# Kernel tuning notes

Hardware: AMD Instinct MI355X
Metric: run time of the kernel (lower is better)

## Reference

```python
import jax, jax.numpy as jnp
import numpy as np
from jax import lax

K_SIZE = 3
STRIDE = 1
PAD = 1
BN_EPS = 1e-5


def _unfold(x, k, stride, pad):
    # x: [B, C, H, W] -> patches [B, L, C*k*k] with torch.unfold feature
    # ordering (channel-major: feat = c*k*k + i*k + j), L = oH*oW
    B, C, H, W = x.shape
    xp = jnp.pad(x, ((0, 0), (0, 0), (pad, pad), (pad, pad)))
    oH = (H + 2 * pad - k) // stride + 1
    oW = (W + 2 * pad - k) // stride + 1
    views = []
    for i in range(k):
        for j in range(k):
            views.append(xp[:, :, i:i + oH * stride:stride, j:j + oW * stride:stride])
    p = jnp.stack(views, axis=0)            # [k*k, B, C, oH, oW]
    p = p.transpose(1, 3, 4, 2, 0)          # [B, oH, oW, C, k*k]
    return p.reshape(B, oH * oW, C * k * k), oH, oW


def _nearest_l1(flat, cents):
    # Online nearest-centroid search under L1, avoids [N, K] x D blowup.
    # flat: [N, D], cents: [K, D] -> int32 indices [N] (first min on ties,
    # matching torch argmin)
    N = flat.shape[0]
    init = (jnp.full((N,), jnp.inf, flat.dtype), jnp.zeros((N,), jnp.int32))
    ks = jnp.arange(cents.shape[0], dtype=jnp.int32)

    def body(carry, kc):
        kidx, c = kc
        d = jnp.abs(flat - c).sum(-1)       # [N]
        bd, bi = carry
        better = d < bd
        return (jnp.where(better, d, bd), jnp.where(better, kidx, bi)), None

    (_, best_idx), _ = lax.scan(body, init, (ks, cents))
    return best_idx


def setup_inputs() -> dict:
    key = jax.random.key(0)
    ks = jax.random.split(key, 5)
    B, Cin, H, W = 8, 64, 56, 56
    K, D, Cout = 256, Cin * K_SIZE * K_SIZE, 128
    return {
        "x": jax.random.normal(ks[0], (B, Cin, H, W), jnp.float32),
        "centroids": jax.random.normal(ks[1], (K, D), jnp.float32),
        "residual_centroids": jax.random.normal(ks[2], (K, D), jnp.float32),
        "dot_centroids": jax.random.normal(ks[3], (K, Cout), jnp.float32),
        "dot_residual_centroids": jax.random.normal(ks[4], (K, Cout), jnp.float32),
        "bn_gamma": jnp.ones((Cout,), jnp.float32),
        "bn_beta": jnp.zeros((Cout,), jnp.float32),
    }


def reference(x, centroids, residual_centroids, dot_centroids,
              dot_residual_centroids, bn_gamma, bn_beta):
    B = x.shape[0]
    Cout = dot_centroids.shape[1]
    patches, oH, oW = _unfold(x, K_SIZE, STRIDE, PAD)   # [B, L, D]
    L, D = patches.shape[1], patches.shape[2]
    flat = patches.reshape(B * L, D)

    # Stage 1: nearest centroid (L1)
    idx1 = _nearest_l1(flat, centroids)                  # [B*L]
    residuals = flat - centroids[idx1]                   # [B*L, D]
    # Stage 2: nearest residual centroid (L1)
    idx2 = _nearest_l1(residuals, residual_centroids)    # [B*L]

    # LUT gather + sum
    out_vals = dot_centroids[idx1] + dot_residual_centroids[idx2]  # [B*L, Cout]
    out = out_vals.reshape(B, L, Cout).transpose(0, 2, 1).reshape(B, Cout, oH, oW)

    # BatchNorm2d (training mode: biased batch statistics)
    mean = out.mean(axis=(0, 2, 3), keepdims=True)
    var = ((out - mean) ** 2).mean(axis=(0, 2, 3), keepdims=True)
    out = (out - mean) * lax.rsqrt(var + BN_EPS)
    out = out * bn_gamma[None, :, None, None] + bn_beta[None, :, None, None]
    return out
```

## Files before the change

### kernel.cpp

```cpp
#include <hip/hip_runtime.h>

#define NP 25088
#define DD 576
#define KC 256

__global__ __launch_bounds__(256) void unfold_kernel(const float* __restrict__ x,
                                                     float* __restrict__ PT) {
  const int d = blockIdx.y;
  const int n = blockIdx.x * 256 + threadIdx.x;
  const int c = d / 9, r = d % 9;
  const int di = r / 3 - 1, dj = r % 3 - 1;
  const int b = n / 3136, hw = n % 3136;
  const int h = hw / 56 + di, w = hw % 56 + dj;
  float v = 0.0f;
  if (h >= 0 && h < 56 && w >= 0 && w < 56)
    v = x[(((size_t)b * 64 + c) * 56 + h) * 56 + w];
  PT[(size_t)d * NP + n] = v;
}

__global__ __launch_bounds__(256) void transpose_kernel(const float* __restrict__ C,
                                                        float* __restrict__ CT) {
  const int d = blockIdx.x;
  const int k = threadIdx.x;
  CT[d * KC + k] = C[k * DD + d];
}

#define ACC4(p, a, s) \
  do { p.x += fabsf(a.x - (s)); p.y += fabsf(a.y - (s)); \
       p.z += fabsf(a.z - (s)); p.w += fabsf(a.w - (s)); } while (0)
#define ADD4(t, p) \
  do { t.x += p.x; t.y += p.y; t.z += p.z; t.w += p.w; } while (0)
#define COMP(v, i) ((i) == 0 ? (v).x : (i) == 1 ? (v).y : (i) == 2 ? (v).z : (v).w)

__global__ __launch_bounds__(256, 5) void nearest_kernel(const float* __restrict__ AT,
                                                         const float* __restrict__ CT,
                                                         float* __restrict__ distc,
                                                         int* __restrict__ idxc) {
  __shared__ float As[2][32][64];
  __shared__ float Bs[2][32][64];

  const int tid = threadIdx.x;
  const int tm = tid >> 4;
  const int tk = tid & 15;
  const int L = blockIdx.x;
  const int xcd = L & 7, r = L >> 3;
  const int mb = xcd * 49 + (r >> 2);
  const int kc = r & 3;
  const int m0 = mb * 64, k0 = kc * 64;

  float4 ra0, ra1, rb0, rb1;
  float4 p0, p1, p2, p3, t0, t1, t2, t3;

  const int frow = tid >> 4, fcol = (tid & 15) * 4;
  const float* ap = AT + (size_t)frow * NP + m0 + fcol;
  const float* bp = CT + frow * KC + k0 + fcol;

#define LOADT() do {                                       \
    ra0 = *(const float4*)(ap);                            \
    ra1 = *(const float4*)(ap + (size_t)16 * NP);          \
    rb0 = *(const float4*)(bp);                            \
    rb1 = *(const float4*)(bp + 16 * KC);                  \
    ap += (size_t)32 * NP; bp += 32 * KC;                  \
  } while (0)

#define WRITET(bf) do {                                    \
    *(float4*)&As[bf][frow][fcol] = ra0;                   \
    *(float4*)&As[bf][16 + frow][fcol] = ra1;              \
    *(float4*)&Bs[bf][frow][fcol] = rb0;                   \
    *(float4*)&Bs[bf][16 + frow][fcol] = rb1;              \
  } while (0)

  LOADT();
  WRITET(0);
  t0 = t1 = t2 = t3 = make_float4(0.f, 0.f, 0.f, 0.f);

  for (int ch = 0; ch < 18; ++ch) {
    if ((ch & 1) == 0) p0 = p1 = p2 = p3 = make_float4(0.f, 0.f, 0.f, 0.f);
    __syncthreads();
    if (ch < 17) LOADT();
    const int buf = ch & 1;
#pragma unroll 8
    for (int d = 0; d < 32; ++d) {
      const float4 a = *(const float4*)&As[buf][d][tm * 4];
      const float4 b = *(const float4*)&Bs[buf][d][tk * 4];
      ACC4(p0, a, b.x);
      ACC4(p1, a, b.y);
      ACC4(p2, a, b.z);
      ACC4(p3, a, b.w);
    }
    if (ch < 17) WRITET((ch + 1) & 1);
    if (ch & 1) {
      ADD4(t0, p0); ADD4(t1, p1); ADD4(t2, p2); ADD4(t3, p3);
    }
  }

#pragma unroll
  for (int i = 0; i < 4; ++i) {
    const float d0 = COMP(t0, i), d1 = COMP(t1, i), d2 = COMP(t2, i), d3 = COMP(t3, i);
    float bd = d0;
    int bk = k0 + tk * 4;
    if (d1 < bd) { bd = d1; bk = k0 + tk * 4 + 1; }
    if (d2 < bd) { bd = d2; bk = k0 + tk * 4 + 2; }
    if (d3 < bd) { bd = d3; bk = k0 + tk * 4 + 3; }
#pragma unroll
    for (int off = 1; off < 16; off <<= 1) {
      const float od = __shfl_xor(bd, off, 64);
      const int ok = __shfl_xor(bk, off, 64);
      if (od < bd || (od == bd && ok < bk)) { bd = od; bk = ok; }
    }
    if (tk == 0) {
      const int m = m0 + tm * 4 + i;
      distc[(size_t)kc * NP + m] = bd;
      idxc[(size_t)kc * NP + m] = bk;
    }
  }
#undef LOADT
#undef WRITET
}

__global__ __launch_bounds__(256) void combine_kernel(const float* __restrict__ distc,
                                                      const int* __restrict__ idxc,
                                                      int* __restrict__ idx_out) {
  const int n = blockIdx.x * 256 + threadIdx.x;
  if (n >= NP) return;
  float bd = distc[n];
  int bi = idxc[n];
#pragma unroll
  for (int s = 1; s < 4; ++s) {
    const float d = distc[(size_t)s * NP + n];
    if (d < bd) { bd = d; bi = idxc[(size_t)s * NP + n]; }
  }
  idx_out[n] = bi;
}

__global__ __launch_bounds__(256) void resid_kernel(float* __restrict__ PT,
                                                    const float* __restrict__ C1T,
                                                    const int* __restrict__ idx1) {
  const int d = blockIdx.y;
  const int n = blockIdx.x * 256 + threadIdx.x;
  const int k = idx1[n];
  PT[(size_t)d * NP + n] -= C1T[d * KC + k];
}

__global__ __launch_bounds__(256) void stats_kernel(const int* __restrict__ idx1,
                                                    const int* __restrict__ idx2,
                                                    const float* __restrict__ dotc,
                                                    const float* __restrict__ dotrc,
                                                    float* __restrict__ gsum,
                                                    float* __restrict__ gsq) {
  __shared__ float ssum[4][128], ssq[4][128];
  const int tid = threadIdx.x, lane = tid & 63, wv = tid >> 6;
  const int wid = blockIdx.x * 4 + wv;
  float s0 = 0.f, s1 = 0.f, q0 = 0.f, q1 = 0.f;
  for (int n = wid; n < NP; n += 512) {
    const int k1 = idx1[n], k2 = idx2[n];
    const float2 u = ((const float2*)(dotc + (size_t)k1 * 128))[lane];
    const float2 v = ((const float2*)(dotrc + (size_t)k2 * 128))[lane];
    const float x0 = u.x + v.x, x1 = u.y + v.y;
    s0 += x0; s1 += x1; q0 += x0 * x0; q1 += x1 * x1;
  }
  ssum[wv][lane * 2] = s0; ssum[wv][lane * 2 + 1] = s1;
  ssq[wv][lane * 2] = q0;  ssq[wv][lane * 2 + 1] = q1;
  __syncthreads();
  if (tid < 128) {
    const float s = ssum[0][tid] + ssum[1][tid] + ssum[2][tid] + ssum[3][tid];
    const float q = ssq[0][tid] + ssq[1][tid] + ssq[2][tid] + ssq[3][tid];
    atomicAdd(&gsum[tid], s);
    atomicAdd(&gsq[tid], q);
  }
}

__global__ void finalize_kernel(const float* __restrict__ gsum,
                                const float* __restrict__ gsq,
                                const float* __restrict__ gamma,
                                const float* __restrict__ beta,
                                float* __restrict__ scalev,
                                float* __restrict__ shiftv) {
  const int c = threadIdx.x;
  const float mean = gsum[c] * (1.0f / NP);
  const float var = gsq[c] * (1.0f / NP) - mean * mean;
  const float inv = rsqrtf(var + 1e-5f);
  const float sc = gamma[c] * inv;
  scalev[c] = sc;
  shiftv[c] = beta[c] - mean * sc;
}

__global__ __launch_bounds__(256) void output_kernel(const int* __restrict__ idx1,
                                                     const int* __restrict__ idx2,
                                                     const float* __restrict__ dotc,
                                                     const float* __restrict__ dotrc,
                                                     const float* __restrict__ scalev,
                                                     const float* __restrict__ shiftv,
                                                     float* __restrict__ out) {
  __shared__ float vals[64][128];
  const int tid = threadIdx.x, lane = tid & 63, wv = tid >> 6;
  const int blk = blockIdx.x;
  const int b = blk / 49, hw0 = (blk % 49) * 64;
  const int n0 = b * 3136 + hw0;
  const float sc0 = scalev[lane * 2], sc1 = scalev[lane * 2 + 1];
  const float sh0 = shiftv[lane * 2], sh1 = shiftv[lane * 2 + 1];
  for (int t = 0; t < 16; ++t) {
    const int nn = wv * 16 + t;
    const int n = n0 + nn;
    const int k1 = idx1[n], k2 = idx2[n];
    const float2 u = ((const float2*)(dotc + (size_t)k1 * 128))[lane];
    const float2 v = ((const float2*)(dotrc + (size_t)k2 * 128))[lane];
    *(float2*)&vals[nn][lane * 2] =
        make_float2(sc0 * (u.x + v.x) + sh0, sc1 * (u.y + v.y) + sh1);
  }
  __syncthreads();
  const int c = tid >> 1, half = tid & 1;
  float* op = out + ((size_t)b * 128 + c) * 3136 + hw0 + half * 32;
#pragma unroll
  for (int i = 0; i < 32; i += 4) {
    float4 w4;
    w4.x = vals[half * 32 + i + 0][c];
    w4.y = vals[half * 32 + i + 1][c];
    w4.z = vals[half * 32 + i + 2][c];
    w4.w = vals[half * 32 + i + 3][c];
    *(float4*)(op + i) = w4;
  }
}

extern "C" void kernel_launch(void* const* d_in, const int* in_sizes, int n_in,
                              void* d_out, int out_size, void* d_ws, size_t ws_size,
                              hipStream_t stream) {
  const float* x     = (const float*)d_in[0];
  const float* cent  = (const float*)d_in[1];
  const float* rcent = (const float*)d_in[2];
  const float* dotc  = (const float*)d_in[3];
  const float* dotrc = (const float*)d_in[4];
  const float* gamma = (const float*)d_in[5];
  const float* beta  = (const float*)d_in[6];
  float* out = (float*)d_out;

  float* PT  = (float*)d_ws;
  float* C1T = PT + (size_t)DD * NP;
  float* C2T = C1T + (size_t)DD * KC;
  int* idx1  = (int*)(C2T + (size_t)DD * KC);
  int* idx2  = idx1 + NP;
  float* distc = (float*)(idx2 + NP);
  int* idxc    = (int*)(distc + 4 * NP);
  float* gsum   = (float*)(idxc + 4 * NP);
  float* gsq    = gsum + 128;
  float* scalev = gsq + 128;
  float* shiftv = scalev + 128;

  unfold_kernel<<<dim3(98, 576), 256, 0, stream>>>(x, PT);
  transpose_kernel<<<576, 256, 0, stream>>>(cent, C1T);
  transpose_kernel<<<576, 256, 0, stream>>>(rcent, C2T);
  nearest_kernel<<<1568, 256, 0, stream>>>(PT, C1T, distc, idxc);
  combine_kernel<<<98, 256, 0, stream>>>(distc, idxc, idx1);
  resid_kernel<<<dim3(98, 576), 256, 0, stream>>>(PT, C1T, idx1);
  nearest_kernel<<<1568, 256, 0, stream>>>(PT, C2T, distc, idxc);
  combine_kernel<<<98, 256, 0, stream>>>(distc, idxc, idx2);
  hipMemsetAsync(gsum, 0, 256 * sizeof(float), stream);
  stats_kernel<<<128, 256, 0, stream>>>(idx1, idx2, dotc, dotrc, gsum, gsq);
  finalize_kernel<<<1, 128, 0, stream>>>(gsum, gsq, gamma, beta, scalev, shiftv);
  output_kernel<<<392, 256, 0, stream>>>(idx1, idx2, dotc, dotrc, scalev, shiftv, out);
}
```

Baseline: 589.7 us.

## Widen nearest-centroid tile to 128 centroids per block, halve centroid splits

Each block of the L1 nearest-centroid kernel now covers 64 points by 128 centroids instead of 64, so each thread computes 8 centroid columns per A load. The grid halves to 784 blocks and the partial-result combine now merges only two splits. The aim is to halve the A-tile reloads from global and LDS per distance computed and to improve arithmetic intensity. The cost is more registers (launch bounds lowered to 3 waves), larger shared memory and fewer blocks, which reduces occupancy.

```diff
diff --git a/kernel.cpp b/kernel.cpp
--- a/kernel.cpp
+++ b/kernel.cpp
@@ -32,76 +32,94 @@
   do { t.x += p.x; t.y += p.y; t.z += p.z; t.w += p.w; } while (0)
 #define COMP(v, i) ((i) == 0 ? (v).x : (i) == 1 ? (v).y : (i) == 2 ? (v).z : (v).w)
 
-__global__ __launch_bounds__(256, 5) void nearest_kernel(const float* __restrict__ AT,
+__global__ __launch_bounds__(256, 3) void nearest_kernel(const float* __restrict__ AT,
                                                          const float* __restrict__ CT,
                                                          float* __restrict__ distc,
                                                          int* __restrict__ idxc) {
   __shared__ float As[2][32][64];
-  __shared__ float Bs[2][32][64];
+  __shared__ float Bs[2][32][128];
 
   const int tid = threadIdx.x;
   const int tm = tid >> 4;
   const int tk = tid & 15;
   const int L = blockIdx.x;
   const int xcd = L & 7, r = L >> 3;
-  const int mb = xcd * 49 + (r >> 2);
-  const int kc = r & 3;
-  const int m0 = mb * 64, k0 = kc * 64;
-
-  float4 ra0, ra1, rb0, rb1;
-  float4 p0, p1, p2, p3, t0, t1, t2, t3;
-
-  const int frow = tid >> 4, fcol = (tid & 15) * 4;
-  const float* ap = AT + (size_t)frow * NP + m0 + fcol;
-  const float* bp = CT + frow * KC + k0 + fcol;
+  const int mb = xcd * 49 + (r >> 1);
+  const int kc = r & 1;
+  const int m0 = mb * 64, k0 = kc * 128;
+
+  float4 ra0, ra1, rb0, rb1, rb2, rb3;
+  float4 p0, p1, p2, p3, p4, p5, p6, p7;
+  float4 t0, t1, t2, t3, t4, t5, t6, t7;
+
+  const int arow = tid >> 4, acol = (tid & 15) * 4;
+  const int brow = tid >> 5, bcol = (tid & 31) * 4;
+  const float* ap = AT + (size_t)arow * NP + m0 + acol;
+  const float* bp = CT + (size_t)brow * KC + k0 + bcol;
 
 #define LOADT() do {                                       \
     ra0 = *(const float4*)(ap);                            \
     ra1 = *(const float4*)(ap + (size_t)16 * NP);          \
     rb0 = *(const float4*)(bp);                            \
-    rb1 = *(const float4*)(bp + 16 * KC);                  \
+    rb1 = *(const float4*)(bp + 8 * KC);                   \
+    rb2 = *(const float4*)(bp + 16 * KC);                  \
+    rb3 = *(const float4*)(bp + 24 * KC);                  \
     ap += (size_t)32 * NP; bp += 32 * KC;                  \
   } while (0)
 
 #define WRITET(bf) do {                                    \
-    *(float4*)&As[bf][frow][fcol] = ra0;                   \
-    *(float4*)&As[bf][16 + frow][fcol] = ra1;              \
-    *(float4*)&Bs[bf][frow][fcol] = rb0;                   \
-    *(float4*)&Bs[bf][16 + frow][fcol] = rb1;              \
+    *(float4*)&As[bf][arow][acol] = ra0;                   \
+    *(float4*)&As[bf][16 + arow][acol] = ra1;              \
+    *(float4*)&Bs[bf][brow][bcol] = rb0;                   \
+    *(float4*)&Bs[bf][8 + brow][bcol] = rb1;               \
+    *(float4*)&Bs[bf][16 + brow][bcol] = rb2;              \
+    *(float4*)&Bs[bf][24 + brow][bcol] = rb3;              \
   } while (0)
 
   LOADT();
   WRITET(0);
-  t0 = t1 = t2 = t3 = make_float4(0.f, 0.f, 0.f, 0.f);
+  t0 = t1 = t2 = t3 = t4 = t5 = t6 = t7 = make_float4(0.f, 0.f, 0.f, 0.f);
 
   for (int ch = 0; ch < 18; ++ch) {
-    if ((ch & 1) == 0) p0 = p1 = p2 = p3 = make_float4(0.f, 0.f, 0.f, 0.f);
+    if ((ch & 1) == 0)
+      p0 = p1 = p2 = p3 = p4 = p5 = p6 = p7 = make_float4(0.f, 0.f, 0.f, 0.f);
     __syncthreads();
     if (ch < 17) LOADT();
-    const int buf = ch & 1;
-#pragma unroll 8
+    const float (*__restrict__ Asb)[64]  = As[ch & 1];
+    const float (*__restrict__ Bsb)[128] = Bs[ch & 1];
+#pragma unroll 4
     for (int d = 0; d < 32; ++d) {
-      const float4 a = *(const float4*)&As[buf][d][tm * 4];
-      const float4 b = *(const float4*)&Bs[buf][d][tk * 4];
+      const float4 a = *(const float4*)&Asb[d][tm * 4];
+      const float4 b = *(const float4*)&Bsb[d][tk * 4];
+      const float4 c = *(const float4*)&Bsb[d][64 + tk * 4];
       ACC4(p0, a, b.x);
       ACC4(p1, a, b.y);
       ACC4(p2, a, b.z);
       ACC4(p3, a, b.w);
+      ACC4(p4, a, c.x);
+      ACC4(p5, a, c.y);
+      ACC4(p6, a, c.z);
+      ACC4(p7, a, c.w);
     }
     if (ch < 17) WRITET((ch + 1) & 1);
     if (ch & 1) {
       ADD4(t0, p0); ADD4(t1, p1); ADD4(t2, p2); ADD4(t3, p3);
+      ADD4(t4, p4); ADD4(t5, p5); ADD4(t6, p6); ADD4(t7, p7);
     }
   }
 
 #pragma unroll
   for (int i = 0; i < 4; ++i) {
-    const float d0 = COMP(t0, i), d1 = COMP(t1, i), d2 = COMP(t2, i), d3 = COMP(t3, i);
-    float bd = d0;
+    float bd = COMP(t0, i);
     int bk = k0 + tk * 4;
-    if (d1 < bd) { bd = d1; bk = k0 + tk * 4 + 1; }
-    if (d2 < bd) { bd = d2; bk = k0 + tk * 4 + 2; }
-    if (d3 < bd) { bd = d3; bk = k0 + tk * 4 + 3; }
+    float dj;
+    dj = COMP(t1, i); if (dj < bd) { bd = dj; bk = k0 + tk * 4 + 1; }
+    dj = COMP(t2, i); if (dj < bd) { bd = dj; bk = k0 + tk * 4 + 2; }
+    dj = COMP(t3, i); if (dj < bd) { bd = dj; bk = k0 + tk * 4 + 3; }
+    dj = COMP(t4, i); if (dj < bd) { bd = dj; bk = k0 + 64 + tk * 4; }
+    dj = COMP(t5, i); if (dj < bd) { bd = dj; bk = k0 + 64 + tk * 4 + 1; }
+    dj = COMP(t6, i); if (dj < bd) { bd = dj; bk = k0 + 64 + tk * 4 + 2; }
+    dj = COMP(t7, i); if (dj < bd) { bd = dj; bk = k0 + 64 + tk * 4 + 3; }
 #pragma unroll
     for (int off = 1; off < 16; off <<= 1) {
       const float od = __shfl_xor(bd, off, 64);
@@ -123,14 +141,8 @@
                                                       int* __restrict__ idx_out) {
   const int n = blockIdx.x * 256 + threadIdx.x;
   if (n >= NP) return;
-  float bd = distc[n];
-  int bi = idxc[n];
-#pragma unroll
-  for (int s = 1; s < 4; ++s) {
-    const float d = distc[(size_t)s * NP + n];
-    if (d < bd) { bd = d; bi = idxc[(size_t)s * NP + n]; }
-  }
-  idx_out[n] = bi;
+  const float d0 = distc[n], d1 = distc[NP + n];
+  idx_out[n] = (d1 < d0) ? idxc[NP + n] : idxc[n];
 }
 
 __global__ __launch_bounds__(256) void resid_kernel(float* __restrict__ PT,
@@ -240,8 +252,8 @@
   int* idx1  = (int*)(C2T + (size_t)DD * KC);
   int* idx2  = idx1 + NP;
   float* distc = (float*)(idx2 + NP);
-  int* idxc    = (int*)(distc + 4 * NP);
-  float* gsum   = (float*)(idxc + 4 * NP);
+  int* idxc    = (int*)(distc + 2 * NP);
+  float* gsum   = (float*)(idxc + 2 * NP);
   float* gsq    = gsum + 128;
   float* scalev = gsq + 128;
   float* shiftv = scalev + 128;
@@ -249,10 +261,10 @@
   unfold_kernel<<<dim3(98, 576), 256, 0, stream>>>(x, PT);
   transpose_kernel<<<576, 256, 0, stream>>>(cent, C1T);
   transpose_kernel<<<576, 256, 0, stream>>>(rcent, C2T);
-  nearest_kernel<<<1568, 256, 0, stream>>>(PT, C1T, distc, idxc);
+  nearest_kernel<<<784, 256, 0, stream>>>(PT, C1T, distc, idxc);
   combine_kernel<<<98, 256, 0, stream>>>(distc, idxc, idx1);
   resid_kernel<<<dim3(98, 576), 256, 0, stream>>>(PT, C1T, idx1);
-  nearest_kernel<<<1568, 256, 0, stream>>>(PT, C2T, distc, idxc);
+  nearest_kernel<<<784, 256, 0, stream>>>(PT, C2T, distc, idxc);
   combine_kernel<<<98, 256, 0, stream>>>(distc, idxc, idx2);
   hipMemsetAsync(gsum, 0, 256 * sizeof(float), stream);
   stats_kernel<<<128, 256, 0, stream>>>(idx1, idx2, dotc, dotrc, gsum, gsq);
```

Measured after the change: 663.0 us. +12.4%, slower.
